# Optimization experiments

Measured on AMD Instinct MI355X. Metric: run time of the kernel, lower is better.

Reference implementation:

```python
import jax, jax.numpy as jnp
import numpy as np

B, NIN, NOUT, K = 1024, 126, 126, 3
H1, H2 = 256, 256

def _linear_params(key, out_f, in_f):
    # torch nn.Linear default init: U(-1/sqrt(in_f), 1/sqrt(in_f))
    bound = 1.0 / np.sqrt(in_f)
    kw, kb = jax.random.split(key)
    W = jax.random.uniform(kw, (out_f, in_f), minval=-bound, maxval=bound, dtype=jnp.float32)
    b = jax.random.uniform(kb, (out_f,), minval=-bound, maxval=bound, dtype=jnp.float32)
    return W, b

def setup_inputs() -> dict:
    key = jax.random.key(0)
    k0, k1, k2, kx, ki, ko = jax.random.split(key, 6)
    W0, b0 = _linear_params(k0, H1, NIN)
    W1, b1 = _linear_params(k1, H2, H1)
    W2, b2 = _linear_params(k2, NOUT, H2)
    x = jax.random.normal(kx, (B, NIN), dtype=jnp.float32)
    batch_in_index = jax.random.randint(ki, (B, NIN, K), 0, NIN + 1)   # NIN is zero-pad row
    batch_out_index = jax.random.randint(ko, (B, NOUT, K), 0, NOUT + 1)  # NOUT is zero-pad row
    return dict(x=x, W0=W0, b0=b0, W1=W1, b1=b1, W2=W2, b2=b2,
                batch_in_index=batch_in_index, batch_out_index=batch_out_index)

def reference(x, W0, b0, W1, b1, W2, b2, batch_in_index, batch_out_index):
    # --- layer 0: BatchIndexedLinear with batch_in_index ---
    # padded weight: (nin+1, h1), last row zeros
    pw0 = jnp.concatenate([W0.T, jnp.zeros((1, W0.shape[0]), W0.dtype)], axis=0)
    bw0 = pw0[batch_in_index].sum(-2)                 # (B, nin, h1)
    h = jnp.einsum('bi,bio->bo', x, bw0) + b0          # (B, h1)
    h = jax.nn.elu(h)
    # --- layer 1: plain linear ---
    h = jax.nn.elu(h @ W1.T + b1)                      # (B, h2)
    # --- layer 2: BatchIndexedLinear with batch_out_index ---
    pw2 = jnp.concatenate([W2, jnp.zeros((1, W2.shape[1]), W2.dtype)], axis=0)  # (nout+1, h2)
    g = pw2[batch_out_index].sum(-2)                   # (B, nout, h2)
    pb2 = jnp.concatenate([b2, jnp.zeros((1,), b2.dtype)])
    bb = pb2[batch_out_index].sum(-1)                  # (B, nout)
    return jnp.einsum('bh,boh->bo', h, g) + bb         # (B, nout)
```

## Files before the change

kernel.cpp:

```cpp
#include <hip/hip_runtime.h>

#define B_    1024
#define NIN_  126
#define NOUT_ 126
#define K_    3
#define H1_   256
#define H2_   256
#define RPB   4
#define TPB   512

__device__ __forceinline__ float elu1(float v) { return v > 0.0f ? v : expm1f(v); }

template<int CTRL>
__device__ __forceinline__ float dpp_add(float v) {
    int s = __builtin_amdgcn_update_dpp(0, __float_as_int(v), CTRL, 0xF, 0xF, true);
    return v + __int_as_float(s);
}
__device__ __forceinline__ float qsum8(float v) {
    v = dpp_add<0xB1>(v);
    v = dpp_add<0x4E>(v);
    int s = __builtin_amdgcn_ds_swizzle(__float_as_int(v), 0x101F);
    return v + __int_as_float(s);
}

__device__ __forceinline__ void barrier_lds() {
    asm volatile("s_waitcnt lgkmcnt(0)\n\ts_barrier" ::: "memory");
}

__global__ __launch_bounds__(TPB) void bim_fused(
    const float* __restrict__ x,  const float* __restrict__ W0,
    const float* __restrict__ b0, const float* __restrict__ W1,
    const float* __restrict__ b1, const float* __restrict__ W2,
    const float* __restrict__ b2, const int*  __restrict__ iidx,
    const int*  __restrict__ oidx, float* __restrict__ out)
{
    __shared__ float xe [RPB][128];
    __shared__ float h1s[RPB][H1_];
    __shared__ float h2s[RPB][H2_];
    __shared__ float ts [RPB][128];

    const int tid  = threadIdx.x;
    const int row0 = blockIdx.x * RPB;
    const int q    = tid & 7;
    const int g    = tid >> 3;

    int aj0, aj1, aj2, ar0, ar1, ar2; float ax0, ax1, ax2;
    {
        const int n0 = tid;
        ar0 = n0 / (NIN_ * K_); const int m0 = n0 - ar0 * (NIN_ * K_);
        aj0 = iidx[(row0 + ar0) * (NIN_ * K_) + m0];
        ax0 = x[(row0 + ar0) * NIN_ + m0 / K_];
        const int n1 = tid + TPB;
        ar1 = n1 / (NIN_ * K_); const int m1 = n1 - ar1 * (NIN_ * K_);
        aj1 = iidx[(row0 + ar1) * (NIN_ * K_) + m1];
        ax1 = x[(row0 + ar1) * NIN_ + m1 / K_];
        const int n2 = tid + 2 * TPB;
        const int n2c = n2 < RPB * NIN_ * K_ ? n2 : 0;
        ar2 = n2c / (NIN_ * K_); const int m2 = n2c - ar2 * (NIN_ * K_);
        aj2 = iidx[(row0 + ar2) * (NIN_ * K_) + m2];
        ax2 = x[(row0 + ar2) * NIN_ + m2 / K_];
        if (n2 >= RPB * NIN_ * K_) aj2 = NIN_;
    }
    int ej0, ej1, ej2;
    {
        const int t = tid < RPB * NOUT_ ? tid : 0;
        const int r = t / NOUT_, o = t - r * NOUT_;
        const int base = (row0 + r) * (NOUT_ * K_) + o * K_;
        ej0 = oidx[base]; ej1 = oidx[base + 1]; ej2 = oidx[base + 2];
    }
    const float4 b0v = *reinterpret_cast<const float4*>(b0 + g * 4);
    const float4 b1v = *reinterpret_cast<const float4*>(b1 + g * 4);
    const int    gD  = (g < 63) ? g : 0;
    const float2 b2v = *reinterpret_cast<const float2*>(b2 + gD * 2);

    const float* wb = W0 + (g * 4) * NIN_;
    float2 wA[4], wB[4];
    {
        const int j = q * 4;
        const int j2 = (j + 2 > NIN_ - 2) ? (NIN_ - 2) : (j + 2);
        #pragma unroll
        for (int oo = 0; oo < 4; ++oo) {
            wA[oo] = *reinterpret_cast<const float2*>(wb + oo * NIN_ + j);
            wB[oo] = *reinterpret_cast<const float2*>(wb + oo * NIN_ + j2);
        }
    }

    (&xe[0][0])[tid] = 0.0f;
    barrier_lds();
    if (aj0 < NIN_) atomicAdd(&xe[ar0][aj0], ax0);
    if (aj1 < NIN_) atomicAdd(&xe[ar1][aj1], ax1);
    if (aj2 < NIN_) atomicAdd(&xe[ar2][aj2], ax2);
    barrier_lds();

    const float* wcp = W1 + (g * 4) * H1_ + q * 4;
    float4 wc[4];
    {
        float acc[4][4] = {};
        #pragma unroll
        for (int jj = 0; jj < 4; ++jj) {
            float2 nA[4], nB[4];
            if (jj < 3) {
                const int j = q * 4 + (jj + 1) * 32;
                const int j2 = (j + 2 > NIN_ - 2) ? (NIN_ - 2) : (j + 2);
                #pragma unroll
                for (int oo = 0; oo < 4; ++oo) {
                    nA[oo] = *reinterpret_cast<const float2*>(wb + oo * NIN_ + j);
                    nB[oo] = *reinterpret_cast<const float2*>(wb + oo * NIN_ + j2);
                }
            }
            const int j = q * 4 + jj * 32;
            float4 a[RPB];
            #pragma unroll
            for (int r = 0; r < RPB; ++r)
                a[r] = *reinterpret_cast<const float4*>(&xe[r][j]);
            #pragma unroll
            for (int oo = 0; oo < 4; ++oo)
                #pragma unroll
                for (int r = 0; r < RPB; ++r) {
                    acc[oo][r] = fmaf(wA[oo].x, a[r].x, acc[oo][r]);
                    acc[oo][r] = fmaf(wA[oo].y, a[r].y, acc[oo][r]);
                    acc[oo][r] = fmaf(wB[oo].x, a[r].z, acc[oo][r]);
                    acc[oo][r] = fmaf(wB[oo].y, a[r].w, acc[oo][r]);
                }
            if (jj < 3) {
                #pragma unroll
                for (int oo = 0; oo < 4; ++oo) { wA[oo] = nA[oo]; wB[oo] = nB[oo]; }
            }
        }
        #pragma unroll
        for (int oo = 0; oo < 4; ++oo)
            wc[oo] = *reinterpret_cast<const float4*>(wcp + oo * H1_);

        #pragma unroll
        for (int oo = 0; oo < 4; ++oo)
            #pragma unroll
            for (int r = 0; r < RPB; ++r) acc[oo][r] = qsum8(acc[oo][r]);
        float v0 = acc[0][0], v1 = acc[0][1];
        #pragma unroll
        for (int i = 1; i < 8; ++i) {
            v0 = (q == i) ? acc[(2 * i) >> 2][(2 * i) & 3]         : v0;
            v1 = (q == i) ? acc[(2 * i + 1) >> 2][(2 * i + 1) & 3] : v1;
        }
        const int oo = q >> 1, r0 = (q & 1) * 2;
        const float bias = (oo == 0) ? b0v.x : (oo == 1) ? b0v.y : (oo == 2) ? b0v.z : b0v.w;
        const int o = g * 4 + oo;
        h1s[r0][o]     = elu1(v0 + bias);
        h1s[r0 + 1][o] = elu1(v1 + bias);
    }
    barrier_lds();

    const float* wdp = W2 + (gD * 2) * H2_ + q * 4;
    float4 wd[2];
    {
        float acc[4][4] = {};
        #pragma unroll
        for (int jj = 0; jj < 8; ++jj) {
            float4 nc[4];
            if (jj < 7) {
                #pragma unroll
                for (int oo = 0; oo < 4; ++oo)
                    nc[oo] = *reinterpret_cast<const float4*>(wcp + oo * H1_ + (jj + 1) * 32);
            }
            const int j = q * 4 + jj * 32;
            float4 a[RPB];
            #pragma unroll
            for (int r = 0; r < RPB; ++r)
                a[r] = *reinterpret_cast<const float4*>(&h1s[r][j]);
            #pragma unroll
            for (int oo = 0; oo < 4; ++oo)
                #pragma unroll
                for (int r = 0; r < RPB; ++r) {
                    acc[oo][r] = fmaf(wc[oo].x, a[r].x, acc[oo][r]);
                    acc[oo][r] = fmaf(wc[oo].y, a[r].y, acc[oo][r]);
                    acc[oo][r] = fmaf(wc[oo].z, a[r].z, acc[oo][r]);
                    acc[oo][r] = fmaf(wc[oo].w, a[r].w, acc[oo][r]);
                }
            if (jj < 7) {
                #pragma unroll
                for (int oo = 0; oo < 4; ++oo) wc[oo] = nc[oo];
            }
        }
        wd[0] = *reinterpret_cast<const float4*>(wdp);
        wd[1] = *reinterpret_cast<const float4*>(wdp + H2_);

        #pragma unroll
        for (int oo = 0; oo < 4; ++oo)
            #pragma unroll
            for (int r = 0; r < RPB; ++r) acc[oo][r] = qsum8(acc[oo][r]);
        float v0 = acc[0][0], v1 = acc[0][1];
        #pragma unroll
        for (int i = 1; i < 8; ++i) {
            v0 = (q == i) ? acc[(2 * i) >> 2][(2 * i) & 3]         : v0;
            v1 = (q == i) ? acc[(2 * i + 1) >> 2][(2 * i + 1) & 3] : v1;
        }
        const int oo = q >> 1, r0 = (q & 1) * 2;
        const float bias = (oo == 0) ? b1v.x : (oo == 1) ? b1v.y : (oo == 2) ? b1v.z : b1v.w;
        const int o = g * 4 + oo;
        h2s[r0][o]     = elu1(v0 + bias);
        h2s[r0 + 1][o] = elu1(v1 + bias);
    }
    barrier_lds();

    {
        float acc[2][4] = {};
        #pragma unroll
        for (int jj = 0; jj < 8; ++jj) {
            float4 nd[2];
            if (jj < 7) {
                nd[0] = *reinterpret_cast<const float4*>(wdp + (jj + 1) * 32);
                nd[1] = *reinterpret_cast<const float4*>(wdp + H2_ + (jj + 1) * 32);
            }
            const int j = q * 4 + jj * 32;
            float4 a[RPB];
            #pragma unroll
            for (int r = 0; r < RPB; ++r)
                a[r] = *reinterpret_cast<const float4*>(&h2s[r][j]);
            #pragma unroll
            for (int oo = 0; oo < 2; ++oo)
                #pragma unroll
                for (int r = 0; r < RPB; ++r) {
                    acc[oo][r] = fmaf(wd[oo].x, a[r].x, acc[oo][r]);
                    acc[oo][r] = fmaf(wd[oo].y, a[r].y, acc[oo][r]);
                    acc[oo][r] = fmaf(wd[oo].z, a[r].z, acc[oo][r]);
                    acc[oo][r] = fmaf(wd[oo].w, a[r].w, acc[oo][r]);
                }
            if (jj < 7) { wd[0] = nd[0]; wd[1] = nd[1]; }
        }
        #pragma unroll
        for (int oo = 0; oo < 2; ++oo)
            #pragma unroll
            for (int r = 0; r < RPB; ++r) acc[oo][r] = qsum8(acc[oo][r]);
        float v = acc[0][0];
        #pragma unroll
        for (int i = 1; i < 8; ++i) v = (q == i) ? acc[i >> 2][i & 3] : v;
        const int oo = q >> 2, rr = q & 3;
        if (g < 63) ts[rr][g * 2 + oo] = v + (oo ? b2v.y : b2v.x);
        else        ts[rr][126 + oo]   = 0.0f;
    }
    barrier_lds();

    if (tid < RPB * NOUT_) {
        const int r = tid / NOUT_, o = tid - r * NOUT_;
        out[(row0 + r) * NOUT_ + o] = ts[r][ej0] + ts[r][ej1] + ts[r][ej2];
    }
}

extern "C" void kernel_launch(void* const* d_in, const int* in_sizes, int n_in,
                              void* d_out, int out_size, void* d_ws, size_t ws_size,
                              hipStream_t stream) {
    const float* x   = (const float*)d_in[0];
    const float* W0  = (const float*)d_in[1];
    const float* b0  = (const float*)d_in[2];
    const float* W1  = (const float*)d_in[3];
    const float* b1  = (const float*)d_in[4];
    const float* W2  = (const float*)d_in[5];
    const float* b2  = (const float*)d_in[6];
    const int*  iidx = (const int*)d_in[7];
    const int*  oidx = (const int*)d_in[8];
    float* out = (float*)d_out;

    bim_fused<<<B_ / RPB, TPB, 0, stream>>>(x, W0, b0, W1, b1, W2, b2, iidx, oidx, out);
}
```

Measured before the change: 15.83 us.

## Prefetch whole weight slices into registers well ahead of each layer

Loads all of W0's slice into registers up front, and issues W1's first half before the atomic barrier. W1's second half and all of W2 are issued midway through the previous layer's FMAs, instead of double-buffering one 32-column chunk at a time. This aims to hide global-memory latency behind the LDS scatter and compute. It raises register pressure substantially (about 64 float4 values live at once), which could lower occupancy or cause spills.

Measured after the change: 15.62 us. No clear change (-1.3%).

```diff
diff --git a/kernel.cpp b/kernel.cpp
--- a/kernel.cpp
+++ b/kernel.cpp
@@ -61,6 +61,20 @@
         ax2 = x[(row0 + ar2) * NIN_ + m2 / K_];
         if (n2 >= RPB * NIN_ * K_) aj2 = NIN_;
     }
+
+    const float* wb = W0 + (g * 4) * NIN_;
+    float2 wA[4][4], wB[4][4];
+    #pragma unroll
+    for (int jj = 0; jj < 4; ++jj) {
+        const int j  = q * 4 + jj * 32;
+        const int j2 = (j + 2 > NIN_ - 2) ? (NIN_ - 2) : (j + 2);
+        #pragma unroll
+        for (int oo = 0; oo < 4; ++oo) {
+            wA[jj][oo] = *reinterpret_cast<const float2*>(wb + oo * NIN_ + j);
+            wB[jj][oo] = *reinterpret_cast<const float2*>(wb + oo * NIN_ + j2);
+        }
+    }
+
     int ej0, ej1, ej2;
     {
         const int t = tid < RPB * NOUT_ ? tid : 0;
@@ -73,41 +87,26 @@
     const int    gD  = (g < 63) ? g : 0;
     const float2 b2v = *reinterpret_cast<const float2*>(b2 + gD * 2);
 
-    const float* wb = W0 + (g * 4) * NIN_;
-    float2 wA[4], wB[4];
-    {
-        const int j = q * 4;
-        const int j2 = (j + 2 > NIN_ - 2) ? (NIN_ - 2) : (j + 2);
-        #pragma unroll
-        for (int oo = 0; oo < 4; ++oo) {
-            wA[oo] = *reinterpret_cast<const float2*>(wb + oo * NIN_ + j);
-            wB[oo] = *reinterpret_cast<const float2*>(wb + oo * NIN_ + j2);
-        }
-    }
-
     (&xe[0][0])[tid] = 0.0f;
     barrier_lds();
     if (aj0 < NIN_) atomicAdd(&xe[ar0][aj0], ax0);
     if (aj1 < NIN_) atomicAdd(&xe[ar1][aj1], ax1);
     if (aj2 < NIN_) atomicAdd(&xe[ar2][aj2], ax2);
-    barrier_lds();
 
     const float* wcp = W1 + (g * 4) * H1_ + q * 4;
-    float4 wc[4];
+    float4 wc1[4][4];
+    #pragma unroll
+    for (int jj = 0; jj < 4; ++jj)
+        #pragma unroll
+        for (int oo = 0; oo < 4; ++oo)
+            wc1[jj][oo] = *reinterpret_cast<const float4*>(wcp + oo * H1_ + jj * 32);
+    barrier_lds();
+
+    float4 wc2[4][4];
     {
         float acc[4][4] = {};
         #pragma unroll
-        for (int jj = 0; jj < 4; ++jj) {
-            float2 nA[4], nB[4];
-            if (jj < 3) {
-                const int j = q * 4 + (jj + 1) * 32;
-                const int j2 = (j + 2 > NIN_ - 2) ? (NIN_ - 2) : (j + 2);
-                #pragma unroll
-                for (int oo = 0; oo < 4; ++oo) {
-                    nA[oo] = *reinterpret_cast<const float2*>(wb + oo * NIN_ + j);
-                    nB[oo] = *reinterpret_cast<const float2*>(wb + oo * NIN_ + j2);
-                }
-            }
+        for (int jj = 0; jj < 2; ++jj) {
             const int j = q * 4 + jj * 32;
             float4 a[RPB];
             #pragma unroll
@@ -117,20 +116,34 @@
             for (int oo = 0; oo < 4; ++oo)
                 #pragma unroll
                 for (int r = 0; r < RPB; ++r) {
-                    acc[oo][r] = fmaf(wA[oo].x, a[r].x, acc[oo][r]);
-                    acc[oo][r] = fmaf(wA[oo].y, a[r].y, acc[oo][r]);
-                    acc[oo][r] = fmaf(wB[oo].x, a[r].z, acc[oo][r]);
-                    acc[oo][r] = fmaf(wB[oo].y, a[r].w, acc[oo][r]);
-                }
-            if (jj < 3) {
-                #pragma unroll
-                for (int oo = 0; oo < 4; ++oo) { wA[oo] = nA[oo]; wB[oo] = nB[oo]; }
-            }
-        }
-        #pragma unroll
-        for (int oo = 0; oo < 4; ++oo)
-            wc[oo] = *reinterpret_cast<const float4*>(wcp + oo * H1_);
-
+                    acc[oo][r] = fmaf(wA[jj][oo].x, a[r].x, acc[oo][r]);
+                    acc[oo][r] = fmaf(wA[jj][oo].y, a[r].y, acc[oo][r]);
+                    acc[oo][r] = fmaf(wB[jj][oo].x, a[r].z, acc[oo][r]);
+                    acc[oo][r] = fmaf(wB[jj][oo].y, a[r].w, acc[oo][r]);
+                }
+        }
+        #pragma unroll
+        for (int jj = 0; jj < 4; ++jj)
+            #pragma unroll
+            for (int oo = 0; oo < 4; ++oo)
+                wc2[jj][oo] = *reinterpret_cast<const float4*>(wcp + oo * H1_ + (jj + 4) * 32);
+        #pragma unroll
+        for (int jj = 2; jj < 4; ++jj) {
+            const int j = q * 4 + jj * 32;
+            float4 a[RPB];
+            #pragma unroll
+            for (int r = 0; r < RPB; ++r)
+                a[r] = *reinterpret_cast<const float4*>(&xe[r][j]);
+            #pragma unroll
+            for (int oo = 0; oo < 4; ++oo)
+                #pragma unroll
+                for (int r = 0; r < RPB; ++r) {
+                    acc[oo][r] = fmaf(wA[jj][oo].x, a[r].x, acc[oo][r]);
+                    acc[oo][r] = fmaf(wA[jj][oo].y, a[r].y, acc[oo][r]);
+                    acc[oo][r] = fmaf(wB[jj][oo].x, a[r].z, acc[oo][r]);
+                    acc[oo][r] = fmaf(wB[jj][oo].y, a[r].w, acc[oo][r]);
+                }
+        }
         #pragma unroll
         for (int oo = 0; oo < 4; ++oo)
             #pragma unroll
@@ -150,17 +163,12 @@
     barrier_lds();
 
     const float* wdp = W2 + (gD * 2) * H2_ + q * 4;
-    float4 wd[2];
+    float4 wd[8][2];
     {
         float acc[4][4] = {};
         #pragma unroll
-        for (int jj = 0; jj < 8; ++jj) {
-            float4 nc[4];
-            if (jj < 7) {
-                #pragma unroll
-                for (int oo = 0; oo < 4; ++oo)
-                    nc[oo] = *reinterpret_cast<const float4*>(wcp + oo * H1_ + (jj + 1) * 32);
-            }
+        for (int jj = 0; jj < 6; ++jj) {
+            const float4* wrow = (jj < 4) ? wc1[jj] : wc2[jj - 4];
             const int j = q * 4 + jj * 32;
             float4 a[RPB];
             #pragma unroll
@@ -170,19 +178,35 @@
             for (int oo = 0; oo < 4; ++oo)
                 #pragma unroll
                 for (int r = 0; r < RPB; ++r) {
-                    acc[oo][r] = fmaf(wc[oo].x, a[r].x, acc[oo][r]);
-                    acc[oo][r] = fmaf(wc[oo].y, a[r].y, acc[oo][r]);
-                    acc[oo][r] = fmaf(wc[oo].z, a[r].z, acc[oo][r]);
-                    acc[oo][r] = fmaf(wc[oo].w, a[r].w, acc[oo][r]);
-                }
-            if (jj < 7) {
-                #pragma unroll
-                for (int oo = 0; oo < 4; ++oo) wc[oo] = nc[oo];
-            }
-        }
-        wd[0] = *reinterpret_cast<const float4*>(wdp);
-        wd[1] = *reinterpret_cast<const float4*>(wdp + H2_);
-
+                    acc[oo][r] = fmaf(wrow[oo].x, a[r].x, acc[oo][r]);
+                    acc[oo][r] = fmaf(wrow[oo].y, a[r].y, acc[oo][r]);
+                    acc[oo][r] = fmaf(wrow[oo].z, a[r].z, acc[oo][r]);
+                    acc[oo][r] = fmaf(wrow[oo].w, a[r].w, acc[oo][r]);
+                }
+        }
+        #pragma unroll
+        for (int jj = 0; jj < 8; ++jj)
+            #pragma unroll
+            for (int oo = 0; oo < 2; ++oo)
+                wd[jj][oo] = *reinterpret_cast<const float4*>(wdp + oo * H2_ + jj * 32);
+        #pragma unroll
+        for (int jj = 6; jj < 8; ++jj) {
+            const float4* wrow = wc2[jj - 4];
+            const int j = q * 4 + jj * 32;
+            float4 a[RPB];
+            #pragma unroll
+            for (int r = 0; r < RPB; ++r)
+                a[r] = *reinterpret_cast<const float4*>(&h1s[r][j]);
+            #pragma unroll
+            for (int oo = 0; oo < 4; ++oo)
+                #pragma unroll
+                for (int r = 0; r < RPB; ++r) {
+                    acc[oo][r] = fmaf(wrow[oo].x, a[r].x, acc[oo][r]);
+                    acc[oo][r] = fmaf(wrow[oo].y, a[r].y, acc[oo][r]);
+                    acc[oo][r] = fmaf(wrow[oo].z, a[r].z, acc[oo][r]);
+                    acc[oo][r] = fmaf(wrow[oo].w, a[r].w, acc[oo][r]);
+                }
+        }
         #pragma unroll
         for (int oo = 0; oo < 4; ++oo)
             #pragma unroll
@@ -205,11 +229,6 @@
         float acc[2][4] = {};
         #pragma unroll
         for (int jj = 0; jj < 8; ++jj) {
-            float4 nd[2];
-            if (jj < 7) {
-                nd[0] = *reinterpret_cast<const float4*>(wdp + (jj + 1) * 32);
-                nd[1] = *reinterpret_cast<const float4*>(wdp + H2_ + (jj + 1) * 32);
-            }
             const int j = q * 4 + jj * 32;
             float4 a[RPB];
             #pragma unroll
@@ -219,12 +238,11 @@
             for (int oo = 0; oo < 2; ++oo)
                 #pragma unroll
                 for (int r = 0; r < RPB; ++r) {
-                    acc[oo][r] = fmaf(wd[oo].x, a[r].x, acc[oo][r]);
-                    acc[oo][r] = fmaf(wd[oo].y, a[r].y, acc[oo][r]);
-                    acc[oo][r] = fmaf(wd[oo].z, a[r].z, acc[oo][r]);
-                    acc[oo][r] = fmaf(wd[oo].w, a[r].w, acc[oo][r]);
-                }
-            if (jj < 7) { wd[0] = nd[0]; wd[1] = nd[1]; }
+                    acc[oo][r] = fmaf(wd[jj][oo].x, a[r].x, acc[oo][r]);
+                    acc[oo][r] = fmaf(wd[jj][oo].y, a[r].y, acc[oo][r]);
+                    acc[oo][r] = fmaf(wd[jj][oo].z, a[r].z, acc[oo][r]);
+                    acc[oo][r] = fmaf(wd[jj][oo].w, a[r].w, acc[oo][r]);
+                }
         }
         #pragma unroll
         for (int oo = 0; oo < 2; ++oo)
```
